# Optimization experiments

Hardware: AMD Instinct MI355X
Metric: run time of the kernel (lower is better)

## Reference

```python
import jax, jax.numpy as jnp
import numpy as np

B, L = 128, 200
NUM_C, D, M = 10000, 128, 64


def setup_inputs() -> dict:
    key = jax.random.key(0)
    ks = jax.random.split(key, 16)
    n = lambda k, s, sc=0.05: jax.random.normal(k, s, dtype=jnp.float32) * sc
    return {
        "q": jax.random.randint(ks[0], (B, L), 0, NUM_C),
        "r": jax.random.randint(ks[1], (B, L), 0, 2),
        "k_emb": n(ks[2], (NUM_C, D)),
        "v_emb": n(ks[3], (2, D)),
        "Mk": n(ks[4], (M, D), 0.2),   # kaiming_normal_
        "Mv0": n(ks[5], (M, D), 0.2),  # kaiming_normal_
        "f_W": n(ks[6], (D, 2 * D)), "f_b": jnp.zeros((D,), jnp.float32),
        "e_W": n(ks[7], (D, D)), "e_b": jnp.zeros((D,), jnp.float32),
        "a_W": n(ks[8], (D, D)), "a_b": jnp.zeros((D,), jnp.float32),
        "ab_W": n(ks[9], (1, D)), "ab_b": jnp.zeros((1,), jnp.float32),
        "df_W": n(ks[10], (1, D)), "df_b": jnp.zeros((1,), jnp.float32),
    }


def reference(q, r, k_emb, v_emb, Mk, Mv0, f_W, f_b, e_W, e_b, a_W, a_b, ab_W, ab_b, df_W, df_b):
    # Embeddings
    k = k_emb[q]                # [B, L, D] question key embedding
    v = k + v_emb[r]            # [B, L, D] value embedding

    # Attention over memory slots, erase/add gates
    w = jax.nn.softmax(jnp.einsum('bld,md->blm', k, Mk), axis=-1)   # [B, L, M]
    e = jax.nn.sigmoid(jnp.einsum('bld,ed->ble', v, e_W) + e_b)      # erase [B, L, D]
    a = jnp.tanh(jnp.einsum('bld,ed->ble', v, a_W) + a_b)            # add   [B, L, D]

    Mvt0 = jnp.broadcast_to(Mv0[None], (q.shape[0], Mv0.shape[0], Mv0.shape[1]))  # [B, M, D]

    def step(Mvt, inp):
        wt, et, at = inp  # [B,M], [B,D], [B,D]
        # read uses memory BEFORE this timestep's write (Mv[:, :-1] in torch)
        read = jnp.einsum('bm,bmd->bd', wt, Mvt)
        we = wt[:, :, None]
        Mvt_new = Mvt * (1.0 - we * et[:, None, :]) + we * at[:, None, :]
        return Mvt_new, read

    _, reads = jax.lax.scan(
        step, Mvt0,
        (w.transpose(1, 0, 2), e.transpose(1, 0, 2), a.transpose(1, 0, 2)))
    reads = reads.transpose(1, 0, 2)  # [B, L, D]

    f = jnp.tanh(jnp.concatenate([reads, k], axis=-1) @ f_W.T + f_b)  # [B, L, D]
    stu_ability = jnp.tanh(f @ ab_W.T + ab_b)   # [B, L, 1] (dropout is identity in eval)
    que_diff = jnp.tanh(k @ df_W.T + df_b)      # [B, L, 1]
    p = jax.nn.sigmoid(3.0 * stu_ability - que_diff)
    return p.squeeze(-1)  # [B, L]
```

## Files before the change

kernel.cpp:

```cpp
#include <hip/hip_runtime.h>

typedef unsigned short ushort_t;
typedef short bf16x8 __attribute__((ext_vector_type(8)));
typedef float f32x4 __attribute__((ext_vector_type(4)));

#define B_ 128
#define L_ 200
#define D_ 128
#define M_ 64

__device__ __forceinline__ float fast_sigmoid(float x) {
    return 1.f / (1.f + __expf(-x));
}

__device__ __forceinline__ float fast_tanh(float x) {
    float xc = fminf(fmaxf(x, -15.f), 15.f);
    float e = __expf(2.f * xc);
    return (e - 1.f) / (e + 1.f);
}

__device__ __forceinline__ ushort_t f2bf(float f) {
    union { float f; unsigned int u; } x;
    x.f = f;
    unsigned int u = x.u;
    unsigned int r = (u + 0x7FFFu + ((u >> 16) & 1u)) >> 16;
    return (ushort_t)r;
}

__device__ __forceinline__ uint4 pack8(float4 a, float4 b) {
    uint4 u;
    u.x = (unsigned)f2bf(a.x) | ((unsigned)f2bf(a.y) << 16);
    u.y = (unsigned)f2bf(a.z) | ((unsigned)f2bf(a.w) << 16);
    u.z = (unsigned)f2bf(b.x) | ((unsigned)f2bf(b.y) << 16);
    u.w = (unsigned)f2bf(b.z) | ((unsigned)f2bf(b.w) << 16);
    return u;
}

#define F_WQ   0u
#define F_EAQ  1638400u
#define F_FKQ  8192000u
#define F_RD   11468800u
#define F_DIFF 14745600u
#define F_PACK 14771200u
#define WPACK_N 57344
#define FPACK_N 16384

__global__ __launch_bounds__(256) void k_pack(
    const float* __restrict__ Mk, const float* __restrict__ eW,
    const float* __restrict__ aW, const float* __restrict__ fW,
    ushort_t* __restrict__ Wpack, ushort_t* __restrict__ Fpack)
{
    int i = blockIdx.x * 256 + threadIdx.x;
    if (i < WPACK_N) {
        int g = i >> 9, lane = (i >> 3) & 63, j = i & 7;
        int nt = g >> 2, ks = g & 3;
        int col = nt * 16 + (lane & 15);
        int d = ks * 32 + ((lane >> 4) << 3) + j;
        float v;
        if (col < 64)       v = Mk[col * 128 + d];
        else if (col < 192) v = eW[(col - 64) * 128 + d];
        else if (col < 320) v = aW[(col - 192) * 128 + d];
        else                v = fW[(col - 320) * 256 + 128 + d];
        Wpack[i] = f2bf(v);
    } else if (i < WPACK_N + FPACK_N) {
        int e = i - WPACK_N;
        int g = e >> 9, lane = (e >> 3) & 63, j = e & 7;
        int nt = g >> 2, ks = g & 3;
        int col = nt * 16 + (lane & 15);
        int d = ks * 32 + ((lane >> 4) << 3) + j;
        Fpack[e] = f2bf(fW[col * 256 + d]);
    }
}

__device__ __forceinline__ void loadB4(const ushort_t* __restrict__ base,
                                       int nt, int lane, bf16x8* b) {
    const ushort_t* p = base + (nt * 256 + lane) * 8;
    b[0] = *(const bf16x8*)(p);
    b[1] = *(const bf16x8*)(p + 512);
    b[2] = *(const bf16x8*)(p + 1024);
    b[3] = *(const bf16x8*)(p + 1536);
}

__global__ __launch_bounds__(256) void k_pre_mfma(
    const int* __restrict__ q, const int* __restrict__ r,
    const float* __restrict__ k_emb, const float* __restrict__ v_emb,
    const ushort_t* __restrict__ Wpack,
    const float* __restrict__ e_b, const float* __restrict__ a_b,
    const float* __restrict__ df_W, const float* __restrict__ df_b,
    float* __restrict__ wq, float* __restrict__ eaq,
    float* __restrict__ fkq, float* __restrict__ diffq)
{
    __shared__ ushort_t sA[8192];
    __shared__ float slog[64 * 68];

    const int tid = threadIdx.x;
    const int pos0 = (blockIdx.x >> 1) * 64;
    const int ng = blockIdx.x & 1;
    const int wave = tid >> 6;
    const int lane = tid & 63;

    #pragma unroll
    for (int i = 0; i < 4; i++) {
        int E = tid + 256 * i;
        int mtile = E >> 8, ks = (E >> 6) & 3, le = E & 63;
        int prow = pos0 + mtile * 16 + (le & 15);
        int dof = ks * 32 + ((le >> 4) << 3);
        int qv = q[prow];
        const float4* kp = (const float4*)(k_emb + qv * 128 + dof);
        float4 ka = kp[0], kb = kp[1];
        if (ng == 0) {
            *(uint4*)&sA[E * 8] = pack8(ka, kb);
        } else {
            int rv = r[prow];
            const float4* vp = (const float4*)(v_emb + rv * 128 + dof);
            float4 va = vp[0], vb = vp[1];
            float4 s0, s1;
            s0.x = ka.x + va.x; s0.y = ka.y + va.y; s0.z = ka.z + va.z; s0.w = ka.w + va.w;
            s1.x = kb.x + vb.x; s1.y = kb.y + vb.y; s1.z = kb.z + vb.z; s1.w = kb.w + vb.w;
            *(uint4*)&sA[E * 8] = pack8(s0, s1);
        }
    }
    __syncthreads();

    bf16x8 A[4];
    #pragma unroll
    for (int ks = 0; ks < 4; ks++)
        A[ks] = *(bf16x8*)&sA[((wave * 4 + ks) * 64 + lane) * 8];

    const int col = lane & 15;
    const int quad = lane >> 4;
    const int rbase = wave * 16 + quad * 4;

    if (ng == 0) {
        bf16x8 Bb[2][4];
        loadB4(Wpack, 0, lane, Bb[0]);
        #pragma unroll
        for (int j = 0; j < 12; j++) {
            if (j < 11) {
                int jn = j + 1;
                loadB4(Wpack, (jn < 4) ? jn : jn + 16, lane, Bb[jn & 1]);
            }
            f32x4 acc = {0.f, 0.f, 0.f, 0.f};
            #pragma unroll
            for (int ks = 0; ks < 4; ks++)
                acc = __builtin_amdgcn_mfma_f32_16x16x32_bf16(A[ks], Bb[j & 1][ks], acc, 0, 0, 0);
            if (j < 4) {
                #pragma unroll
                for (int reg = 0; reg < 4; reg++)
                    slog[(rbase + reg) * 68 + j * 16 + col] = acc[reg];
            } else {
                int c = (j - 4) * 16 + col;
                #pragma unroll
                for (int reg = 0; reg < 4; reg++)
                    fkq[(pos0 + rbase + reg) * 128 + c] = acc[reg];
            }
        }

        {
            int row = tid >> 2, ln = tid & 3;
            int pos = pos0 + row;
            int qv = q[pos];
            const float4* kp = (const float4*)(k_emb + qv * 128) + ln * 8;
            const float4* dfp = (const float4*)df_W + ln * 8;
            float s = 0.f;
            #pragma unroll
            for (int j = 0; j < 8; j++) {
                float4 a = kp[j], b = dfp[j];
                s = fmaf(a.x, b.x, fmaf(a.y, b.y, fmaf(a.z, b.z, fmaf(a.w, b.w, s))));
            }
            s += __shfl_xor(s, 1); s += __shfl_xor(s, 2);
            if (ln == 0) diffq[pos] = fast_tanh(s + df_b[0]);
        }

        __syncthreads();

        {
            int row = tid >> 2, ln = tid & 3;
            const float* lr = slog + row * 68 + ln * 16;
            float v[16];
            #pragma unroll
            for (int j = 0; j < 16; j++) v[j] = lr[j];
            float mx = v[0];
            #pragma unroll
            for (int j = 1; j < 16; j++) mx = fmaxf(mx, v[j]);
            mx = fmaxf(mx, __shfl_xor(mx, 1));
            mx = fmaxf(mx, __shfl_xor(mx, 2));
            float s = 0.f;
            #pragma unroll
            for (int j = 0; j < 16; j++) { v[j] = __expf(v[j] - mx); s += v[j]; }
            s += __shfl_xor(s, 1); s += __shfl_xor(s, 2);
            float inv = 1.f / s;
            float* wout = wq + (pos0 + row) * 64 + ln * 16;
            #pragma unroll
            for (int j = 0; j < 16; j++) wout[j] = v[j] * inv;
        }
    } else {
        bf16x8 Be[2][4], Ba[2][4];
        loadB4(Wpack, 4, lane, Be[0]);
        loadB4(Wpack, 12, lane, Ba[0]);
        #pragma unroll
        for (int i = 0; i < 8; i++) {
            if (i < 7) {
                loadB4(Wpack, 5 + i, lane, Be[(i + 1) & 1]);
                loadB4(Wpack, 13 + i, lane, Ba[(i + 1) & 1]);
            }
            f32x4 ae = {0.f, 0.f, 0.f, 0.f};
            f32x4 aa = {0.f, 0.f, 0.f, 0.f};
            #pragma unroll
            for (int ks = 0; ks < 4; ks++) {
                ae = __builtin_amdgcn_mfma_f32_16x16x32_bf16(A[ks], Be[i & 1][ks], ae, 0, 0, 0);
                aa = __builtin_amdgcn_mfma_f32_16x16x32_bf16(A[ks], Ba[i & 1][ks], aa, 0, 0, 0);
            }
            int c = i * 16 + col;
            float ebv = e_b[c], abv = a_b[c];
            #pragma unroll
            for (int reg = 0; reg < 4; reg++) {
                float2 o;
                o.x = fast_sigmoid(ae[reg] + ebv);
                o.y = fast_tanh(aa[reg] + abv);
                *(float2*)(eaq + ((pos0 + rbase + reg) * 128 + c) * 2) = o;
            }
        }
    }
}

__global__ __launch_bounds__(256) void k_scan(
    const float* __restrict__ wq, const float* __restrict__ eaq,
    const float* __restrict__ Mv0, float* __restrict__ reads)
{
    __shared__ float w_lds[2][512];
    __shared__ float ea_lds[2][512];

    const int tid = threadIdx.x;
    const int b = blockIdx.x >> 2;
    const int dq = (blockIdx.x & 3) * 32;
    const int s = tid & 7;
    const int dl = tid >> 3;
    const int d = dq + dl;

    float Mv[8];
    #pragma unroll
    for (int j = 0; j < 8; j++) Mv[j] = Mv0[(s * 8 + j) * D_ + d];

    const float* wbase = wq + b * (L_ * M_);
    const float* eabase = eaq + b * (L_ * 256) + dq * 2;
    float* rrow = reads + b * (L_ * D_) + d;

    const bool is_w = (tid < 128);
    const int li = is_w ? tid : (tid - 128);
    const int ett = li >> 4;
    const int ejj = (li & 15) * 4;

    {
        float4 st;
        if (is_w) st = *(const float4*)(wbase + li * 4);
        else      st = *(const float4*)(eabase + ett * 256 + ejj);
        float* dst = is_w ? &w_lds[0][li * 4] : &ea_lds[0][li * 4];
        *(float4*)dst = st;
    }
    __syncthreads();

    int buf = 0;
    for (int c = 0; c < 25; c++) {
        const int t0 = c * 8;
        float4 nst;
        if (c < 24) {
            if (is_w) nst = *(const float4*)(wbase + (t0 + 8) * 64 + li * 4);
            else      nst = *(const float4*)(eabase + (t0 + 8 + ett) * 256 + ejj);
        }
        #pragma unroll
        for (int tt = 0; tt < 8; tt++) {
            float4 wa = *(const float4*)&w_lds[buf][tt * 64 + s * 8];
            float4 wb = *(const float4*)&w_lds[buf][tt * 64 + s * 8 + 4];
            float2 ea = *(const float2*)&ea_lds[buf][tt * 64 + dl * 2];
            float ev = ea.x, av = ea.y, ne = -ev;
            float r0 = wa.x * Mv[0];
            float r1 = wa.y * Mv[1];
            r0 = fmaf(wa.z, Mv[2], r0); r1 = fmaf(wa.w, Mv[3], r1);
            r0 = fmaf(wb.x, Mv[4], r0); r1 = fmaf(wb.y, Mv[5], r1);
            r0 = fmaf(wb.z, Mv[6], r0); r1 = fmaf(wb.w, Mv[7], r1);
            Mv[0] = fmaf(wa.x, fmaf(ne, Mv[0], av), Mv[0]);
            Mv[1] = fmaf(wa.y, fmaf(ne, Mv[1], av), Mv[1]);
            Mv[2] = fmaf(wa.z, fmaf(ne, Mv[2], av), Mv[2]);
            Mv[3] = fmaf(wa.w, fmaf(ne, Mv[3], av), Mv[3]);
            Mv[4] = fmaf(wb.x, fmaf(ne, Mv[4], av), Mv[4]);
            Mv[5] = fmaf(wb.y, fmaf(ne, Mv[5], av), Mv[5]);
            Mv[6] = fmaf(wb.z, fmaf(ne, Mv[6], av), Mv[6]);
            Mv[7] = fmaf(wb.w, fmaf(ne, Mv[7], av), Mv[7]);
            float rd = r0 + r1;
            rd += __shfl_xor(rd, 1);
            rd += __shfl_xor(rd, 2);
            rd += __shfl_xor(rd, 4);
            if (s == 0) rrow[(t0 + tt) * D_] = rd;
        }
        if (c < 24) {
            float* dst = is_w ? &w_lds[buf ^ 1][li * 4] : &ea_lds[buf ^ 1][li * 4];
            *(float4*)dst = nst;
        }
        __syncthreads();
        buf ^= 1;
    }
}

__global__ __launch_bounds__(512) void k_final_mfma(
    const float* __restrict__ reads, const float* __restrict__ fkq,
    const float* __restrict__ diffq, const ushort_t* __restrict__ Fpack,
    const float* __restrict__ f_b, const float* __restrict__ ab_W,
    const float* __restrict__ ab_b, float* __restrict__ out)
{
    __shared__ ushort_t srA[8192];
    __shared__ float sab[64 * 2];

    const int tid = threadIdx.x;
    const int pos0 = blockIdx.x * 64;
    const int wave = tid >> 6;
    const int lane = tid & 63;
    const int mt = wave & 3;
    const int half = wave >> 2;

    #pragma unroll
    for (int i = 0; i < 2; i++) {
        int E = tid + 512 * i;
        int mtile = E >> 8, ks = (E >> 6) & 3, le = E & 63;
        int prow = pos0 + mtile * 16 + (le & 15);
        int dof = ks * 32 + ((le >> 4) << 3);
        const float4* rp = (const float4*)(reads + prow * 128 + dof);
        *(uint4*)&srA[E * 8] = pack8(rp[0], rp[1]);
    }
    __syncthreads();

    bf16x8 A[4];
    #pragma unroll
    for (int ks = 0; ks < 4; ks++)
        A[ks] = *(bf16x8*)&srA[((mt * 4 + ks) * 64 + lane) * 8];

    const int col = lane & 15;
    const int quad = lane >> 4;
    const int rbase = mt * 16 + quad * 4;

    float abacc[4] = {0.f, 0.f, 0.f, 0.f};

    bf16x8 Bb[2][4];
    loadB4(Fpack, half * 4, lane, Bb[0]);
    #pragma unroll
    for (int i = 0; i < 4; i++) {
        if (i < 3) loadB4(Fpack, half * 4 + i + 1, lane, Bb[(i + 1) & 1]);
        f32x4 acc = {0.f, 0.f, 0.f, 0.f};
        #pragma unroll
        for (int ks = 0; ks < 4; ks++)
            acc = __builtin_amdgcn_mfma_f32_16x16x32_bf16(A[ks], Bb[i & 1][ks], acc, 0, 0, 0);
        int c = (half * 4 + i) * 16 + col;
        float fb = f_b[c];
        float abw = ab_W[c];
        #pragma unroll
        for (int reg = 0; reg < 4; reg++) {
            float fv = fast_tanh(acc[reg] + fkq[(pos0 + rbase + reg) * 128 + c] + fb);
            abacc[reg] = fmaf(abw, fv, abacc[reg]);
        }
    }

    #pragma unroll
    for (int reg = 0; reg < 4; reg++) {
        float v = abacc[reg];
        v += __shfl_xor(v, 1); v += __shfl_xor(v, 2);
        v += __shfl_xor(v, 4); v += __shfl_xor(v, 8);
        abacc[reg] = v;
    }
    if (col == 0) {
        #pragma unroll
        for (int reg = 0; reg < 4; reg++)
            sab[(rbase + reg) * 2 + half] = abacc[reg];
    }
    __syncthreads();
    if (tid < 64) {
        float ab = fast_tanh(sab[tid * 2] + sab[tid * 2 + 1] + ab_b[0]);
        int pos = pos0 + tid;
        out[pos] = fast_sigmoid(3.f * ab - diffq[pos]);
    }
}

extern "C" void kernel_launch(void* const* d_in, const int* in_sizes, int n_in,
                              void* d_out, int out_size, void* d_ws, size_t ws_size,
                              hipStream_t stream)
{
    const int*   q     = (const int*)d_in[0];
    const int*   r     = (const int*)d_in[1];
    const float* k_emb = (const float*)d_in[2];
    const float* v_emb = (const float*)d_in[3];
    const float* Mk    = (const float*)d_in[4];
    const float* Mv0   = (const float*)d_in[5];
    const float* f_W   = (const float*)d_in[6];
    const float* f_b   = (const float*)d_in[7];
    const float* e_W   = (const float*)d_in[8];
    const float* e_b   = (const float*)d_in[9];
    const float* a_W   = (const float*)d_in[10];
    const float* a_b   = (const float*)d_in[11];
    const float* ab_W  = (const float*)d_in[12];
    const float* ab_b  = (const float*)d_in[13];
    const float* df_W  = (const float*)d_in[14];
    const float* df_b  = (const float*)d_in[15];

    float* ws = (float*)d_ws;
    float* out = (float*)d_out;
    ushort_t* Wpack = (ushort_t*)(ws + F_PACK);
    ushort_t* Fpack = Wpack + WPACK_N;

    k_pack<<<288, 256, 0, stream>>>(Mk, e_W, a_W, f_W, Wpack, Fpack);

    k_pre_mfma<<<800, 256, 0, stream>>>(
        q, r, k_emb, v_emb, Wpack, e_b, a_b, df_W, df_b,
        ws + F_WQ, ws + F_EAQ, ws + F_FKQ, ws + F_DIFF);

    k_scan<<<512, 256, 0, stream>>>(
        ws + F_WQ, ws + F_EAQ, Mv0, ws + F_RD);

    k_final_mfma<<<400, 512, 0, stream>>>(
        ws + F_RD, ws + F_FKQ, ws + F_DIFF, Fpack,
        f_b, ab_W, ab_b, out);
}
```

Measured before the change: 165.8 us.

## Restructure memory scan to wave-per-slot-group with LDS cross-wave read reduction

Rewrites the scan kernel so each block handles half of D for one batch row, and each wave owns 16 memory slots per d column, with one lane per d. Attention weights and erase/add values now come straight from global memory through wave-uniform and per-lane loads, replacing the LDS double-buffered staging. Partial reads are summed across the four waves in LDS instead of by shuffle reduction. The grid drops from 512 to 256 blocks, so each thread runs longer serial chains with fewer blocks in flight, and global load latency now sits on the recurrence's critical path.

Result: faster. 160.2 us (-3.4%).

```diff
diff --git a/kernel.cpp b/kernel.cpp
--- a/kernel.cpp
+++ b/kernel.cpp
@@ -228,77 +228,72 @@
     const float* __restrict__ wq, const float* __restrict__ eaq,
     const float* __restrict__ Mv0, float* __restrict__ reads)
 {
-    __shared__ float w_lds[2][512];
-    __shared__ float ea_lds[2][512];
+    __shared__ float pbuf[2][4][8][64];
 
     const int tid = threadIdx.x;
-    const int b = blockIdx.x >> 2;
-    const int dq = (blockIdx.x & 3) * 32;
-    const int s = tid & 7;
-    const int dl = tid >> 3;
-    const int d = dq + dl;
-
-    float Mv[8];
-    #pragma unroll
-    for (int j = 0; j < 8; j++) Mv[j] = Mv0[(s * 8 + j) * D_ + d];
-
-    const float* wbase = wq + b * (L_ * M_);
-    const float* eabase = eaq + b * (L_ * 256) + dq * 2;
-    float* rrow = reads + b * (L_ * D_) + d;
-
-    const bool is_w = (tid < 128);
-    const int li = is_w ? tid : (tid - 128);
-    const int ett = li >> 4;
-    const int ejj = (li & 15) * 4;
-
-    {
-        float4 st;
-        if (is_w) st = *(const float4*)(wbase + li * 4);
-        else      st = *(const float4*)(eabase + ett * 256 + ejj);
-        float* dst = is_w ? &w_lds[0][li * 4] : &ea_lds[0][li * 4];
-        *(float4*)dst = st;
-    }
-    __syncthreads();
-
-    int buf = 0;
+    const int b = blockIdx.x >> 1;
+    const int dh = blockIdx.x & 1;
+    const int sc = __builtin_amdgcn_readfirstlane(tid >> 6);
+    const int lane = tid & 63;
+    const int d = dh * 64 + lane;
+
+    float Mv[16];
+    #pragma unroll
+    for (int j = 0; j < 16; j++) Mv[j] = Mv0[(sc * 16 + j) * D_ + d];
+
+    const float4* wbase = (const float4*)(wq + b * (L_ * M_) + sc * 16);
+    const float2* eabase = (const float2*)(eaq + b * (L_ * 256)) + d;
+    float* rbase = reads + b * (L_ * D_) + dh * 64;
+
+    const int rtt = tid >> 6;
+    const int rdd = tid & 63;
+
     for (int c = 0; c < 25; c++) {
         const int t0 = c * 8;
-        float4 nst;
-        if (c < 24) {
-            if (is_w) nst = *(const float4*)(wbase + (t0 + 8) * 64 + li * 4);
-            else      nst = *(const float4*)(eabase + (t0 + 8 + ett) * 256 + ejj);
-        }
+        const int bb = c & 1;
         #pragma unroll
         for (int tt = 0; tt < 8; tt++) {
-            float4 wa = *(const float4*)&w_lds[buf][tt * 64 + s * 8];
-            float4 wb = *(const float4*)&w_lds[buf][tt * 64 + s * 8 + 4];
-            float2 ea = *(const float2*)&ea_lds[buf][tt * 64 + dl * 2];
+            const float4* wp = wbase + (t0 + tt) * 16;
+            float4 w0 = wp[0], w1 = wp[1], w2 = wp[2], w3 = wp[3];
+            float2 ea = eabase[(t0 + tt) * 128];
             float ev = ea.x, av = ea.y, ne = -ev;
-            float r0 = wa.x * Mv[0];
-            float r1 = wa.y * Mv[1];
-            r0 = fmaf(wa.z, Mv[2], r0); r1 = fmaf(wa.w, Mv[3], r1);
-            r0 = fmaf(wb.x, Mv[4], r0); r1 = fmaf(wb.y, Mv[5], r1);
-            r0 = fmaf(wb.z, Mv[6], r0); r1 = fmaf(wb.w, Mv[7], r1);
-            Mv[0] = fmaf(wa.x, fmaf(ne, Mv[0], av), Mv[0]);
-            Mv[1] = fmaf(wa.y, fmaf(ne, Mv[1], av), Mv[1]);
-            Mv[2] = fmaf(wa.z, fmaf(ne, Mv[2], av), Mv[2]);
-            Mv[3] = fmaf(wa.w, fmaf(ne, Mv[3], av), Mv[3]);
-            Mv[4] = fmaf(wb.x, fmaf(ne, Mv[4], av), Mv[4]);
-            Mv[5] = fmaf(wb.y, fmaf(ne, Mv[5], av), Mv[5]);
-            Mv[6] = fmaf(wb.z, fmaf(ne, Mv[6], av), Mv[6]);
-            Mv[7] = fmaf(wb.w, fmaf(ne, Mv[7], av), Mv[7]);
-            float rd = r0 + r1;
-            rd += __shfl_xor(rd, 1);
-            rd += __shfl_xor(rd, 2);
-            rd += __shfl_xor(rd, 4);
-            if (s == 0) rrow[(t0 + tt) * D_] = rd;
-        }
-        if (c < 24) {
-            float* dst = is_w ? &w_lds[buf ^ 1][li * 4] : &ea_lds[buf ^ 1][li * 4];
-            *(float4*)dst = nst;
+            float r0, r1;
+            r0 = w0.x * Mv[0];
+            r1 = w0.y * Mv[1];
+            r0 = fmaf(w0.z, Mv[2], r0);  r1 = fmaf(w0.w, Mv[3], r1);
+            r0 = fmaf(w1.x, Mv[4], r0);  r1 = fmaf(w1.y, Mv[5], r1);
+            r0 = fmaf(w1.z, Mv[6], r0);  r1 = fmaf(w1.w, Mv[7], r1);
+            r0 = fmaf(w2.x, Mv[8], r0);  r1 = fmaf(w2.y, Mv[9], r1);
+            r0 = fmaf(w2.z, Mv[10], r0); r1 = fmaf(w2.w, Mv[11], r1);
+            r0 = fmaf(w3.x, Mv[12], r0); r1 = fmaf(w3.y, Mv[13], r1);
+            r0 = fmaf(w3.z, Mv[14], r0); r1 = fmaf(w3.w, Mv[15], r1);
+            Mv[0]  = fmaf(w0.x, fmaf(ne, Mv[0],  av), Mv[0]);
+            Mv[1]  = fmaf(w0.y, fmaf(ne, Mv[1],  av), Mv[1]);
+            Mv[2]  = fmaf(w0.z, fmaf(ne, Mv[2],  av), Mv[2]);
+            Mv[3]  = fmaf(w0.w, fmaf(ne, Mv[3],  av), Mv[3]);
+            Mv[4]  = fmaf(w1.x, fmaf(ne, Mv[4],  av), Mv[4]);
+            Mv[5]  = fmaf(w1.y, fmaf(ne, Mv[5],  av), Mv[5]);
+            Mv[6]  = fmaf(w1.z, fmaf(ne, Mv[6],  av), Mv[6]);
+            Mv[7]  = fmaf(w1.w, fmaf(ne, Mv[7],  av), Mv[7]);
+            Mv[8]  = fmaf(w2.x, fmaf(ne, Mv[8],  av), Mv[8]);
+            Mv[9]  = fmaf(w2.y, fmaf(ne, Mv[9],  av), Mv[9]);
+            Mv[10] = fmaf(w2.z, fmaf(ne, Mv[10], av), Mv[10]);
+            Mv[11] = fmaf(w2.w, fmaf(ne, Mv[11], av), Mv[11]);
+            Mv[12] = fmaf(w3.x, fmaf(ne, Mv[12], av), Mv[12]);
+            Mv[13] = fmaf(w3.y, fmaf(ne, Mv[13], av), Mv[13]);
+            Mv[14] = fmaf(w3.z, fmaf(ne, Mv[14], av), Mv[14]);
+            Mv[15] = fmaf(w3.w, fmaf(ne, Mv[15], av), Mv[15]);
+            pbuf[bb][sc][tt][lane] = r0 + r1;
         }
         __syncthreads();
-        buf ^= 1;
+        {
+            float s0 = pbuf[bb][0][rtt][rdd] + pbuf[bb][1][rtt][rdd]
+                     + pbuf[bb][2][rtt][rdd] + pbuf[bb][3][rtt][rdd];
+            float s1 = pbuf[bb][0][rtt + 4][rdd] + pbuf[bb][1][rtt + 4][rdd]
+                     + pbuf[bb][2][rtt + 4][rdd] + pbuf[bb][3][rtt + 4][rdd];
+            rbase[(t0 + rtt) * D_ + rdd] = s0;
+            rbase[(t0 + rtt + 4) * D_ + rdd] = s1;
+        }
     }
 }
 
@@ -411,7 +406,7 @@
         q, r, k_emb, v_emb, Wpack, e_b, a_b, df_W, df_b,
         ws + F_WQ, ws + F_EAQ, ws + F_FKQ, ws + F_DIFF);
 
-    k_scan<<<512, 256, 0, stream>>>(
+    k_scan<<<256, 256, 0, stream>>>(
         ws + F_WQ, ws + F_EAQ, Mv0, ws + F_RD);
 
     k_final_mfma<<<400, 512, 0, stream>>>(
```
